# Kernel optimization log

Hardware: AMD Instinct MI355X
Metric: run time of the kernel (lower is better)

The kernel has to match this reference:

```python
import jax, jax.numpy as jnp
import numpy as np

EMBED_DIM = 1024
NUM_HEADS = 16
D_K = EMBED_DIM // NUM_HEADS  # 64 quantum wires per head


def setup_inputs() -> dict:
    key = jax.random.key(0)
    k1, k2, k3 = jax.random.split(key, 3)
    x = jax.random.normal(k1, (8, 2048, EMBED_DIM), dtype=jnp.float32)
    # single shared projection weight (source creates ONE nn.Linear used for q,k,v and out)
    W = jax.random.normal(k2, (EMBED_DIM, EMBED_DIM), dtype=jnp.float32) * 0.02
    # trainable RY angles, one per wire, shared across tokens and heads
    theta = jax.random.normal(k3, (D_K,), dtype=jnp.float32)
    return {"x": x, "W": W, "theta": theta}


def _quantum_project(h, theta):
    # h: [B, S, E] -> per-head wires [B, S, H, d_k]
    # Circuit per wire i: |0> -> RX(h_i) -> RY(theta_i) -> <Z>
    # Product state closed form: <Z> = cos(theta_i) * cos(h_i)
    B, S, E = h.shape
    hw = h.reshape(B, S, NUM_HEADS, D_K)
    return jnp.cos(theta) * jnp.cos(hw)  # [B, S, H, d_k]


def reference(x, W, theta):
    # one Linear (no bias) shared by q, k, v -> identical projections
    proj = x @ W.T  # [B, S, E]
    qq = _quantum_project(proj, theta)  # == k_q == v_q, [B, S, H, d_k]
    # scores attend heads-vs-heads per token (faithful to source matmul on dims -2,-1)
    scores = jnp.einsum('bshd,bsgd->bshg', qq, qq) / np.sqrt(D_K).astype(np.float32)
    attn = jax.nn.softmax(scores, axis=-1)  # dropout omitted (eval)
    out = jnp.einsum('bshg,bsgd->bshd', attn, qq)  # [B, S, H, d_k]
    B, S = x.shape[0], x.shape[1]
    out = out.reshape(B, S, EMBED_DIM) @ W.T  # output projection with same shared linear
    return out
```

## Files before the change

kernel.cpp:

```cpp
#include <hip/hip_runtime.h>
#include <hip/hip_bf16.h>
#include <stdint.h>

#define NB    8
#define NS    2048
#define NE    1024
#define NH    16
#define NDK   64
#define MTOK  (NB*NS)

typedef __attribute__((ext_vector_type(8))) short bf16x8;
typedef __attribute__((ext_vector_type(4))) float f32x4;

__device__ __forceinline__ ushort f2bf(float f) {
  uint32_t u = __float_as_uint(f);
  u += 0x7FFFu + ((u >> 16) & 1u);
  return (ushort)(u >> 16);
}

__device__ __forceinline__ void gload16(const void* g, void* l) {
  __builtin_amdgcn_global_load_lds(
      (const __attribute__((address_space(1))) void*)g,
      (__attribute__((address_space(3))) void*)l, 16, 0, 0);
}

__global__ __launch_bounds__(256) void cvt_bf16(const float* __restrict__ in,
                                                ushort* __restrict__ out, int n4) {
  int stride = gridDim.x * blockDim.x;
  for (int j = blockIdx.x * blockDim.x + threadIdx.x; j < n4; j += stride) {
    float4 v = ((const float4*)in)[j];
    ushort4 o;
    o.x = f2bf(v.x); o.y = f2bf(v.y); o.z = f2bf(v.z); o.w = f2bf(v.w);
    ((ushort4*)out)[j] = o;
  }
}

#define GM 256
#define GN 256
#define GK 64

template<int EPI>
__global__ __launch_bounds__(512, 2) void gemm256(const ushort* __restrict__ A,
                                                  const ushort* __restrict__ Bm,
                                                  float* __restrict__ Cf,
                                                  ushort* __restrict__ Cq,
                                                  const float* __restrict__ theta,
                                                  int M, int N, int K) {
  __shared__ ushort As[2][GM * GK];
  __shared__ ushort Bs[2][GN * GK];

  const int tid  = threadIdx.x;
  const int wid  = tid >> 6;
  const int lane = tid & 63;
  const int wr   = wid >> 2;
  const int wc   = wid & 3;
  const int fr   = lane & 15;
  const int ks   = lane >> 4;

  int b  = blockIdx.x;
  int wg = ((b & 7) << 5) | (b >> 3);
  int br = wg >> 2, bc = wg & 3;

  const ushort* Abase = A  + (size_t)(br * GM) * K;
  const ushort* Bbase = Bm + (size_t)(bc * GN) * K;

  const int srow = lane >> 3;
  const int sch8 = ((lane & 7) ^ srow) * 8;

  const int sA0 = ((0 + ks) ^ (fr & 7)) * 8;
  const int sA1 = ((4 + ks) ^ (fr & 7)) * 8;

  f32x4 zero = {0.f, 0.f, 0.f, 0.f};
  f32x4 acc[8][4];
#pragma unroll
  for (int mi = 0; mi < 8; ++mi)
#pragma unroll
    for (int ni = 0; ni < 4; ++ni) acc[mi][ni] = zero;

  auto stA = [&](int buf, int mh, int kt) {
#pragma unroll
    for (int j = 0; j < 2; ++j) {
      int rl = mh * 128 + j * 64 + wid * 8;
      gload16(Abase + (size_t)(rl + srow) * K + kt * GK + sch8,
              &As[buf][rl * GK]);
    }
  };
  auto stB = [&](int buf, int mh, int kt) {
#pragma unroll
    for (int j = 0; j < 2; ++j) {
      int rl = mh * 128 + j * 64 + wid * 8;
      gload16(Bbase + (size_t)(rl + srow) * K + kt * GK + sch8,
              &Bs[buf][rl * GK]);
    }
  };

  stB(0, 0, 0); stB(0, 1, 0); stA(0, 0, 0); stA(0, 1, 0);
  asm volatile("s_waitcnt vmcnt(2)" ::: "memory");
  __builtin_amdgcn_s_barrier();

  const int NKT = K / GK;
  int cur = 0;
  for (int t = 0; t < NKT; ++t) {
    const ushort* Ac = As[cur];
    const ushort* Bc = Bs[cur];
    const int nb = cur ^ 1;
    const bool pf = (t + 1 < NKT);
    bf16x8 af[4], bv[4];

#pragma unroll
    for (int mi = 0; mi < 4; ++mi)
      af[mi] = *(const bf16x8*)&Ac[(mi * 32 + wr * 16 + fr) * GK + sA0];
#pragma unroll
    for (int ni = 0; ni < 4; ++ni)
      bv[ni] = *(const bf16x8*)&Bc[(ni * 64 + wc * 16 + fr) * GK + sA0];
    if (pf) { stB(nb, 0, t + 1); stB(nb, 1, t + 1); stA(nb, 0, t + 1); stA(nb, 1, t + 1); }
    __builtin_amdgcn_s_barrier();
    asm volatile("s_waitcnt lgkmcnt(0)" ::: "memory");
    __builtin_amdgcn_sched_barrier(0);
    __builtin_amdgcn_s_setprio(1);
#pragma unroll
    for (int mi = 0; mi < 4; ++mi)
#pragma unroll
      for (int ni = 0; ni < 4; ++ni)
        acc[mi][ni] = __builtin_amdgcn_mfma_f32_16x16x32_bf16(af[mi], bv[ni], acc[mi][ni], 0, 0, 0);
    __builtin_amdgcn_s_setprio(0);
    if (pf) asm volatile("s_waitcnt vmcnt(8)" ::: "memory");
    else    asm volatile("s_waitcnt vmcnt(0)" ::: "memory");
    __builtin_amdgcn_s_barrier();

#pragma unroll
    for (int mi = 0; mi < 4; ++mi)
      af[mi] = *(const bf16x8*)&Ac[((mi + 4) * 32 + wr * 16 + fr) * GK + sA0];
    __builtin_amdgcn_s_barrier();
    asm volatile("s_waitcnt lgkmcnt(0)" ::: "memory");
    __builtin_amdgcn_sched_barrier(0);
    __builtin_amdgcn_s_setprio(1);
#pragma unroll
    for (int mi = 0; mi < 4; ++mi)
#pragma unroll
      for (int ni = 0; ni < 4; ++ni)
        acc[mi + 4][ni] = __builtin_amdgcn_mfma_f32_16x16x32_bf16(af[mi], bv[ni], acc[mi + 4][ni], 0, 0, 0);
    __builtin_amdgcn_s_setprio(0);
    __builtin_amdgcn_s_barrier();

#pragma unroll
    for (int mi = 0; mi < 4; ++mi)
      af[mi] = *(const bf16x8*)&Ac[(mi * 32 + wr * 16 + fr) * GK + sA1];
#pragma unroll
    for (int ni = 0; ni < 4; ++ni)
      bv[ni] = *(const bf16x8*)&Bc[(ni * 64 + wc * 16 + fr) * GK + sA1];
    __builtin_amdgcn_s_barrier();
    asm volatile("s_waitcnt lgkmcnt(0)" ::: "memory");
    __builtin_amdgcn_sched_barrier(0);
    __builtin_amdgcn_s_setprio(1);
#pragma unroll
    for (int mi = 0; mi < 4; ++mi)
#pragma unroll
      for (int ni = 0; ni < 4; ++ni)
        acc[mi][ni] = __builtin_amdgcn_mfma_f32_16x16x32_bf16(af[mi], bv[ni], acc[mi][ni], 0, 0, 0);
    __builtin_amdgcn_s_setprio(0);
    __builtin_amdgcn_s_barrier();

#pragma unroll
    for (int mi = 0; mi < 4; ++mi)
      af[mi] = *(const bf16x8*)&Ac[((mi + 4) * 32 + wr * 16 + fr) * GK + sA1];
    __builtin_amdgcn_s_barrier();
    asm volatile("s_waitcnt lgkmcnt(0)" ::: "memory");
    __builtin_amdgcn_sched_barrier(0);
    __builtin_amdgcn_s_setprio(1);
#pragma unroll
    for (int mi = 0; mi < 4; ++mi)
#pragma unroll
      for (int ni = 0; ni < 4; ++ni)
        acc[mi + 4][ni] = __builtin_amdgcn_mfma_f32_16x16x32_bf16(af[mi], bv[ni], acc[mi + 4][ni], 0, 0, 0);
    __builtin_amdgcn_s_setprio(0);
    if (pf) asm volatile("s_waitcnt vmcnt(2)" ::: "memory");
    __builtin_amdgcn_s_barrier();

    cur ^= 1;
  }

  const int colL = wc * 16 + fr;
  float ct = 0.f;
  if (EPI == 1) ct = __cosf(theta[colL]);
#pragma unroll
  for (int mi = 0; mi < 8; ++mi) {
    int row0 = br * GM + mi * 32 + wr * 16 + ks * 4;
#pragma unroll
    for (int ni = 0; ni < 4; ++ni) {
      size_t cbase = (size_t)row0 * N + bc * GN + ni * 64 + colL;
#pragma unroll
      for (int i = 0; i < 4; ++i) {
        if (EPI == 1)
          Cq[cbase + (size_t)i * N] = f2bf(ct * __cosf(acc[mi][ni][i]));
        else
          Cf[cbase + (size_t)i * N] = acc[mi][ni][i];
      }
    }
  }
}

__global__ __launch_bounds__(256) void attn_quantum(const ushort* __restrict__ qqb,
                                                    ushort* __restrict__ aout) {
  __shared__ ushort T[4][64 * 32];
  int tid = threadIdx.x;
  int wv  = tid >> 6, l = tid & 63;
  size_t tok = (size_t)blockIdx.x * 4 + wv;
  const ushort* src = qqb + tok * NE;
  ushort* Tw = T[wv];

  int h  = l & 15;
  int kb = l >> 4;

  bf16x8 f0 = *(const bf16x8*)(src + h * 64 + kb * 8);
  bf16x8 f1 = *(const bf16x8*)(src + h * 64 + kb * 8 + 32);

#pragma unroll
  for (int jj = 0; jj < 8; ++jj) {
    int d0 = kb * 8 + jj;
    int d1 = d0 + 32;
    Tw[d0 * 32 + (((h >> 3) ^ ((d0 >> 3) & 3)) << 3) + (h & 7)] = (ushort)f0[jj];
    Tw[d1 * 32 + (((h >> 3) ^ ((d1 >> 3) & 3)) << 3) + (h & 7)] = (ushort)f1[jj];
  }

  f32x4 sa = {0.f, 0.f, 0.f, 0.f};
  sa = __builtin_amdgcn_mfma_f32_16x16x32_bf16(f0, f0, sa, 0, 0, 0);
  sa = __builtin_amdgcn_mfma_f32_16x16x32_bf16(f1, f1, sa, 0, 0, 0);

  float s[4];
#pragma unroll
  for (int i = 0; i < 4; ++i) s[i] = sa[i] * 0.125f;

  float mx = fmaxf(fmaxf(s[0], s[1]), fmaxf(s[2], s[3]));
  mx = fmaxf(mx, __shfl_xor(mx, 16));
  mx = fmaxf(mx, __shfl_xor(mx, 32));
  float e[4], sum = 0.f;
#pragma unroll
  for (int i = 0; i < 4; ++i) { e[i] = __expf(s[i] - mx); sum += e[i]; }
  sum += __shfl_xor(sum, 16);
  sum += __shfl_xor(sum, 32);
  float inv = 1.f / sum;
#pragma unroll
  for (int i = 0; i < 4; ++i) e[i] *= inv;

  int s1 = h + (kb & 1) * 32;
  float q1[4], q2[4];
#pragma unroll
  for (int i = 0; i < 4; ++i) {
    q1[i] = __shfl(e[i], s1);
    q2[i] = __shfl(e[i], s1 + 16);
  }
  bool live = (kb < 2);
  bf16x8 pa;
#pragma unroll
  for (int i = 0; i < 4; ++i) {
    pa[i]     = live ? (short)f2bf(q1[i]) : (short)0;
    pa[4 + i] = live ? (short)f2bf(q2[i]) : (short)0;
  }

  __syncthreads();

  f32x4 o[4];
#pragma unroll
  for (int c = 0; c < 4; ++c) {
    int r = c * 16 + h;
    int slot = (kb & 1) ^ ((r >> 3) & 3);
    bf16x8 bfrag = *(const bf16x8*)&Tw[r * 32 + slot * 8];
    f32x4 z = {0.f, 0.f, 0.f, 0.f};
    o[c] = __builtin_amdgcn_mfma_f32_16x16x32_bf16(pa, bfrag, z, 0, 0, 0);
  }

  ushort* dst = aout + tok * NE;
#pragma unroll
  for (int c = 0; c < 4; ++c)
#pragma unroll
    for (int i = 0; i < 4; ++i)
      dst[(kb * 4 + i) * NDK + c * 16 + h] = f2bf(o[c][i]);
}

extern "C" void kernel_launch(void* const* d_in, const int* in_sizes, int n_in,
                              void* d_out, int out_size, void* d_ws, size_t ws_size,
                              hipStream_t stream) {
  const float* x     = (const float*)d_in[0];
  const float* W     = (const float*)d_in[1];
  const float* theta = (const float*)d_in[2];
  float* out = (float*)d_out;

  char* ws = (char*)d_ws;
  ushort* xb  = (ushort*)ws;
  ushort* Wb  = (ushort*)(ws + (size_t)MTOK * NE * 2);
  ushort* qqb = (ushort*)(ws + (size_t)MTOK * NE * 2 + (size_t)NE * NE * 2);
  ushort* aout = xb;

  cvt_bf16<<<1024, 256, 0, stream>>>(x, xb, MTOK * NE / 4);
  cvt_bf16<<<256, 256, 0, stream>>>(W, Wb, NE * NE / 4);

  int nwg = (MTOK / GM) * (NE / GN);
  gemm256<1><<<nwg, 512, 0, stream>>>(xb, Wb, nullptr, qqb, theta, MTOK, NE, NE);

  attn_quantum<<<MTOK / 4, 256, 0, stream>>>(qqb, aout);

  gemm256<0><<<nwg, 512, 0, stream>>>(aout, Wb, out, nullptr, nullptr, MTOK, NE, NE);
}
```

Before: 116.3 us.

## Fuse fp32-to-bf16 conversion of x into first GEMM's A-tile loading

Measured after the change: 204.1 us. +75.5%, slower.

```diff
diff --git a/kernel.cpp b/kernel.cpp
--- a/kernel.cpp
+++ b/kernel.cpp
@@ -38,9 +38,109 @@
 #define GM 256
 #define GN 256
 #define GK 64
-
-template<int EPI>
-__global__ __launch_bounds__(512, 2) void gemm256(const ushort* __restrict__ A,
+#define KC 1024
+#define NKT (KC / GK)
+
+#define LOADA(kt, AR)                                                         \
+  do {                                                                        \
+    _Pragma("unroll")                                                         \
+    for (int j = 0; j < 4; ++j) {                                             \
+      int rl = wid * 32 + j * 8 + srow;                                       \
+      size_t base = (size_t)(br * GM + rl) * (KC / 4) + (kt) * 16 + cs * 2;   \
+      AR[2 * j]     = Af4[base];                                              \
+      AR[2 * j + 1] = Af4[base + 1];                                          \
+    }                                                                         \
+  } while (0)
+
+#define WRITEA(buf, AR)                                                       \
+  do {                                                                        \
+    _Pragma("unroll")                                                         \
+    for (int j = 0; j < 4; ++j) {                                             \
+      int rl = wid * 32 + j * 8 + srow;                                       \
+      bf16x8 v;                                                               \
+      v[0] = (short)f2bf(AR[2*j].x);   v[1] = (short)f2bf(AR[2*j].y);         \
+      v[2] = (short)f2bf(AR[2*j].z);   v[3] = (short)f2bf(AR[2*j].w);         \
+      v[4] = (short)f2bf(AR[2*j+1].x); v[5] = (short)f2bf(AR[2*j+1].y);       \
+      v[6] = (short)f2bf(AR[2*j+1].z); v[7] = (short)f2bf(AR[2*j+1].w);       \
+      *(bf16x8*)&As[buf][rl * GK + wslot] = v;                                \
+    }                                                                         \
+  } while (0)
+
+#define MFMA_QUAD(MOFF)                                                       \
+  __builtin_amdgcn_sched_barrier(0);                                          \
+  __builtin_amdgcn_s_setprio(1);                                              \
+  _Pragma("unroll")                                                           \
+  for (int mi = 0; mi < 4; ++mi)                                              \
+    _Pragma("unroll")                                                         \
+    for (int ni = 0; ni < 4; ++ni)                                            \
+      acc[mi + (MOFF)][ni] = __builtin_amdgcn_mfma_f32_16x16x32_bf16(         \
+          af[mi], bv[ni], acc[mi + (MOFF)][ni], 0, 0, 0);                     \
+  __builtin_amdgcn_s_setprio(0);                                              \
+  __builtin_amdgcn_sched_barrier(0);
+
+#define BODY(T, ARL, ARW)                                                     \
+  {                                                                           \
+    const int t = (T);                                                        \
+    const ushort* Ac = As[cur];                                               \
+    const ushort* Bc = Bs[cur];                                               \
+    const int nb = cur ^ 1;                                                   \
+    const bool pf = (t + 1 < NKT);                                            \
+    bf16x8 af[4], bv[4];                                                      \
+                        \
+    _Pragma("unroll")                                                         \
+    for (int mi = 0; mi < 4; ++mi)                                            \
+      af[mi] = *(const bf16x8*)&Ac[(mi * 32 + wr * 16 + fr) * GK + sA0];      \
+    _Pragma("unroll")                                                         \
+    for (int ni = 0; ni < 4; ++ni)                                            \
+      bv[ni] = *(const bf16x8*)&Bc[(ni * 64 + wc * 16 + fr) * GK + sA0];      \
+    if (pf) {                                                                 \
+      stB(nb, 0, t + 1); stB(nb, 1, t + 1);                                   \
+      if (MODE == 0) { stA(nb, 0, t + 1); stA(nb, 1, t + 1); }                \
+    }                                                                         \
+    if (MODE == 1 && (t + 2) < NKT) LOADA(t + 2, ARL);                        \
+    MFMA_QUAD(0)                                                              \
+    if (MODE == 0) {                                                          \
+      if (pf) asm volatile("s_waitcnt vmcnt(8)" ::: "memory");                \
+      else    asm volatile("s_waitcnt vmcnt(0)" ::: "memory");                \
+    }                                                                         \
+    __builtin_amdgcn_s_barrier();                                             \
+                                              \
+    _Pragma("unroll")                                                         \
+    for (int mi = 0; mi < 4; ++mi)                                            \
+      af[mi] = *(const bf16x8*)&Ac[((mi + 4) * 32 + wr * 16 + fr) * GK + sA0];\
+    MFMA_QUAD(4)                                                              \
+    __builtin_amdgcn_s_barrier();                                             \
+                                              \
+    _Pragma("unroll")                                                         \
+    for (int mi = 0; mi < 4; ++mi)                                            \
+      af[mi] = *(const bf16x8*)&Ac[(mi * 32 + wr * 16 + fr) * GK + sA1];      \
+    _Pragma("unroll")                                                         \
+    for (int ni = 0; ni < 4; ++ni)                                            \
+      bv[ni] = *(const bf16x8*)&Bc[(ni * 64 + wc * 16 + fr) * GK + sA1];      \
+    MFMA_QUAD(0)                                                              \
+    __builtin_amdgcn_s_barrier();                                             \
+                          \
+    _Pragma("unroll")                                                         \
+    for (int mi = 0; mi < 4; ++mi)                                            \
+      af[mi] = *(const bf16x8*)&Ac[((mi + 4) * 32 + wr * 16 + fr) * GK + sA1];\
+    MFMA_QUAD(4)                                                              \
+    if (MODE == 0) {                                                          \
+      if (pf) asm volatile("s_waitcnt vmcnt(2)" ::: "memory");                \
+    } else {                                                                  \
+      if (pf) {                                                               \
+        if ((t + 2) < NKT) asm volatile("s_waitcnt vmcnt(8)" ::: "memory");   \
+        else               asm volatile("s_waitcnt vmcnt(0)" ::: "memory");   \
+        WRITEA(nb, ARW);                                                      \
+        asm volatile("s_waitcnt lgkmcnt(0)" ::: "memory");                    \
+      }                                                                       \
+    }                                                                         \
+    __builtin_amdgcn_s_barrier();                                             \
+    cur ^= 1;                                                                 \
+  }
+
+template<int MODE>
+__global__ __launch_bounds__(512, 2) void gemm256(const ushort* __restrict__ Ab,
+                                                  const float* __restrict__ Af,
                                                   const ushort* __restrict__ Bm,
                                                   float* __restrict__ Cf,
                                                   ushort* __restrict__ Cq,
@@ -61,8 +161,9 @@
   int wg = ((b & 7) << 5) | (b >> 3);
   int br = wg >> 2, bc = wg & 3;
 
-  const ushort* Abase = A  + (size_t)(br * GM) * K;
-  const ushort* Bbase = Bm + (size_t)(bc * GN) * K;
+  const ushort* Bbase = Bm + (size_t)(bc * GN) * KC;
+  const ushort* Abase = (MODE == 0) ? (Ab + (size_t)(br * GM) * KC) : nullptr;
+  const float4* Af4   = (MODE == 1) ? ((const float4*)Af) : nullptr;
 
   const int srow = lane >> 3;
   const int sch8 = ((lane & 7) ^ srow) * 8;
@@ -70,6 +171,9 @@
   const int sA0 = ((0 + ks) ^ (fr & 7)) * 8;
   const int sA1 = ((4 + ks) ^ (fr & 7)) * 8;
 
+  const int cs    = lane & 7;
+  const int wslot = (cs ^ srow) * 8;
+
   f32x4 zero = {0.f, 0.f, 0.f, 0.f};
   f32x4 acc[8][4];
 #pragma unroll
@@ -81,7 +185,7 @@
 #pragma unroll
     for (int j = 0; j < 2; ++j) {
       int rl = mh * 128 + j * 64 + wid * 8;
-      gload16(Abase + (size_t)(rl + srow) * K + kt * GK + sch8,
+      gload16(Abase + (size_t)(rl + srow) * KC + kt * GK + sch8,
               &As[buf][rl * GK]);
     }
   };
@@ -89,100 +193,35 @@
 #pragma unroll
     for (int j = 0; j < 2; ++j) {
       int rl = mh * 128 + j * 64 + wid * 8;
-      gload16(Bbase + (size_t)(rl + srow) * K + kt * GK + sch8,
+      gload16(Bbase + (size_t)(rl + srow) * KC + kt * GK + sch8,
               &Bs[buf][rl * GK]);
     }
   };
 
-  stB(0, 0, 0); stB(0, 1, 0); stA(0, 0, 0); stA(0, 1, 0);
-  asm volatile("s_waitcnt vmcnt(2)" ::: "memory");
+  float4 arP[8], arQ[8];
+
+  stB(0, 0, 0); stB(0, 1, 0);
+  if (MODE == 0) {
+    stA(0, 0, 0); stA(0, 1, 0);
+    asm volatile("s_waitcnt vmcnt(2)" ::: "memory");
+  } else {
+    LOADA(0, arP);
+    asm volatile("s_waitcnt vmcnt(0)" ::: "memory");
+    WRITEA(0, arP);
+    LOADA(1, arP);
+    asm volatile("s_waitcnt lgkmcnt(0)" ::: "memory");
+  }
   __builtin_amdgcn_s_barrier();
 
-  const int NKT = K / GK;
   int cur = 0;
-  for (int t = 0; t < NKT; ++t) {
-    const ushort* Ac = As[cur];
-    const ushort* Bc = Bs[cur];
-    const int nb = cur ^ 1;
-    const bool pf = (t + 1 < NKT);
-    bf16x8 af[4], bv[4];
-
-#pragma unroll
-    for (int mi = 0; mi < 4; ++mi)
-      af[mi] = *(const bf16x8*)&Ac[(mi * 32 + wr * 16 + fr) * GK + sA0];
-#pragma unroll
-    for (int ni = 0; ni < 4; ++ni)
-      bv[ni] = *(const bf16x8*)&Bc[(ni * 64 + wc * 16 + fr) * GK + sA0];
-    if (pf) { stB(nb, 0, t + 1); stB(nb, 1, t + 1); stA(nb, 0, t + 1); stA(nb, 1, t + 1); }
-    __builtin_amdgcn_s_barrier();
-    asm volatile("s_waitcnt lgkmcnt(0)" ::: "memory");
-    __builtin_amdgcn_sched_barrier(0);
-    __builtin_amdgcn_s_setprio(1);
-#pragma unroll
-    for (int mi = 0; mi < 4; ++mi)
-#pragma unroll
-      for (int ni = 0; ni < 4; ++ni)
-        acc[mi][ni] = __builtin_amdgcn_mfma_f32_16x16x32_bf16(af[mi], bv[ni], acc[mi][ni], 0, 0, 0);
-    __builtin_amdgcn_s_setprio(0);
-    if (pf) asm volatile("s_waitcnt vmcnt(8)" ::: "memory");
-    else    asm volatile("s_waitcnt vmcnt(0)" ::: "memory");
-    __builtin_amdgcn_s_barrier();
-
-#pragma unroll
-    for (int mi = 0; mi < 4; ++mi)
-      af[mi] = *(const bf16x8*)&Ac[((mi + 4) * 32 + wr * 16 + fr) * GK + sA0];
-    __builtin_amdgcn_s_barrier();
-    asm volatile("s_waitcnt lgkmcnt(0)" ::: "memory");
-    __builtin_amdgcn_sched_barrier(0);
-    __builtin_amdgcn_s_setprio(1);
-#pragma unroll
-    for (int mi = 0; mi < 4; ++mi)
-#pragma unroll
-      for (int ni = 0; ni < 4; ++ni)
-        acc[mi + 4][ni] = __builtin_amdgcn_mfma_f32_16x16x32_bf16(af[mi], bv[ni], acc[mi + 4][ni], 0, 0, 0);
-    __builtin_amdgcn_s_setprio(0);
-    __builtin_amdgcn_s_barrier();
-
-#pragma unroll
-    for (int mi = 0; mi < 4; ++mi)
-      af[mi] = *(const bf16x8*)&Ac[(mi * 32 + wr * 16 + fr) * GK + sA1];
-#pragma unroll
-    for (int ni = 0; ni < 4; ++ni)
-      bv[ni] = *(const bf16x8*)&Bc[(ni * 64 + wc * 16 + fr) * GK + sA1];
-    __builtin_amdgcn_s_barrier();
-    asm volatile("s_waitcnt lgkmcnt(0)" ::: "memory");
-    __builtin_amdgcn_sched_barrier(0);
-    __builtin_amdgcn_s_setprio(1);
-#pragma unroll
-    for (int mi = 0; mi < 4; ++mi)
-#pragma unroll
-      for (int ni = 0; ni < 4; ++ni)
-        acc[mi][ni] = __builtin_amdgcn_mfma_f32_16x16x32_bf16(af[mi], bv[ni], acc[mi][ni], 0, 0, 0);
-    __builtin_amdgcn_s_setprio(0);
-    __builtin_amdgcn_s_barrier();
-
-#pragma unroll
-    for (int mi = 0; mi < 4; ++mi)
-      af[mi] = *(const bf16x8*)&Ac[((mi + 4) * 32 + wr * 16 + fr) * GK + sA1];
-    __builtin_amdgcn_s_barrier();
-    asm volatile("s_waitcnt lgkmcnt(0)" ::: "memory");
-    __builtin_amdgcn_sched_barrier(0);
-    __builtin_amdgcn_s_setprio(1);
-#pragma unroll
-    for (int mi = 0; mi < 4; ++mi)
-#pragma unroll
-      for (int ni = 0; ni < 4; ++ni)
-        acc[mi + 4][ni] = __builtin_amdgcn_mfma_f32_16x16x32_bf16(af[mi], bv[ni], acc[mi + 4][ni], 0, 0, 0);
-    __builtin_amdgcn_s_setprio(0);
-    if (pf) asm volatile("s_waitcnt vmcnt(2)" ::: "memory");
-    __builtin_amdgcn_s_barrier();
-
-    cur ^= 1;
+  for (int t2 = 0; t2 < NKT; t2 += 2) {
+    BODY(t2,     arQ, arP)
+    BODY(t2 + 1, arP, arQ)
   }
 
   const int colL = wc * 16 + fr;
   float ct = 0.f;
-  if (EPI == 1) ct = __cosf(theta[colL]);
+  if (MODE == 1) ct = __cosf(theta[colL]);
 #pragma unroll
   for (int mi = 0; mi < 8; ++mi) {
     int row0 = br * GM + mi * 32 + wr * 16 + ks * 4;
@@ -191,7 +230,7 @@
       size_t cbase = (size_t)row0 * N + bc * GN + ni * 64 + colL;
 #pragma unroll
       for (int i = 0; i < 4; ++i) {
-        if (EPI == 1)
+        if (MODE == 1)
           Cq[cbase + (size_t)i * N] = f2bf(ct * __cosf(acc[mi][ni][i]));
         else
           Cf[cbase + (size_t)i * N] = acc[mi][ni][i];
@@ -287,18 +326,16 @@
   float* out = (float*)d_out;
 
   char* ws = (char*)d_ws;
-  ushort* xb  = (ushort*)ws;
-  ushort* Wb  = (ushort*)(ws + (size_t)MTOK * NE * 2);
-  ushort* qqb = (ushort*)(ws + (size_t)MTOK * NE * 2 + (size_t)NE * NE * 2);
-  ushort* aout = xb;
-
-  cvt_bf16<<<1024, 256, 0, stream>>>(x, xb, MTOK * NE / 4);
+  ushort* Wb   = (ushort*)ws;
+  ushort* qqb  = (ushort*)(ws + (size_t)NE * NE * 2);
+  ushort* aout = (ushort*)(ws + (size_t)NE * NE * 2 + (size_t)MTOK * NE * 2);
+
   cvt_bf16<<<256, 256, 0, stream>>>(W, Wb, NE * NE / 4);
 
   int nwg = (MTOK / GM) * (NE / GN);
-  gemm256<1><<<nwg, 512, 0, stream>>>(xb, Wb, nullptr, qqb, theta, MTOK, NE, NE);
+  gemm256<1><<<nwg, 512, 0, stream>>>(nullptr, x, Wb, nullptr, qqb, theta, MTOK, NE, NE);
 
   attn_quantum<<<MTOK / 4, 256, 0, stream>>>(qqb, aout);
 
-  gemm256<0><<<nwg, 512, 0, stream>>>(aout, Wb, out, nullptr, nullptr, MTOK, NE, NE);
-}
+  gemm256<0><<<nwg, 512, 0, stream>>>(aout, nullptr, Wb, out, nullptr, nullptr, MTOK, NE, NE);
+}
```
